# Performance work log

Hardware: AMD Instinct MI355X
Metric: run time of the kernel (lower is better)

## Reference

```python
import jax, jax.numpy as jnp
import numpy as np

B, H, W, D, O = 16, 128, 128, 64, 256

def setup_inputs() -> dict:
    key = jax.random.key(0)
    k1, k2 = jax.random.split(key)
    x = jax.random.normal(k1, (B, H, W, D), dtype=jnp.float32)
    omega = jax.random.normal(k2, (O, D), dtype=jnp.float32)  # prototypes, init N(0,1)
    return {"x": x, "omega": omega}

def reference(x, omega):
    # Squared L2 distance from each pixel feature to each prototype,
    x2 = jnp.sum(x * x, axis=-1, keepdims=True)          # [B,H,W,1]
    p2 = jnp.sum(omega * omega, axis=-1)                  # [O]
    xp = jnp.einsum('bhwd,od->bhwo', x, omega)            # [B,H,W,O]
    dist = x2 + p2 - 2.0 * xp                             # [B,H,W,O]
    # original stacks per-prototype [B,H,W,1] slices along dim=3 -> [B,H,W,O,1]
    return dist[..., None]
```

## Files before the change

### kernel.cpp

```cpp
#include <hip/hip_runtime.h>


typedef __attribute__((ext_vector_type(4))) float f32x4;
typedef __attribute__((ext_vector_type(16))) float f32x16;
typedef __attribute__((ext_vector_type(8))) short s16x8;
typedef __attribute__((ext_vector_type(4))) unsigned int u32x4;

constexpr int D_ = 64;
constexpr int O_ = 256;
constexpr int M_ = 16 * 128 * 128;
constexpr int ITERS = 2;
constexpr int PIX_PER_BLOCK = 4 * 32 * ITERS;
constexpr int NBLOCKS = M_ / PIX_PER_BLOCK;

__device__ __forceinline__ unsigned short f2bf(float f) {
    unsigned u = __builtin_bit_cast(unsigned, f);
    u += 0x7FFFu + ((u >> 16) & 1u);
    return (unsigned short)(u >> 16);
}

__global__ __launch_bounds__(256, 4) void dist_kernel(
    const float* __restrict__ x,
    const float* __restrict__ om,
    float* __restrict__ out)
{
    __shared__ u32x4 lfrag[32 * 64];
    __shared__ __align__(16) float lp2[O_];

    const int tid  = threadIdx.x;
    const int wave = tid >> 6;
    const int lane = tid & 63;
    const int p    = lane & 31;
    const int h    = lane >> 5;

#pragma unroll
    for (int tt = 0; tt < 2; ++tt) {
        const int T = wave * 2 + tt;
        float p2p = 0.f;
#pragma unroll
        for (int s = 0; s < 4; ++s) {
            const float* src = om + (T * 32 + p) * D_ + s * 16 + h * 8;
            f32x4 v0 = *(const f32x4*)(src);
            f32x4 v1 = *(const f32x4*)(src + 4);
            s16x8 f;
#pragma unroll
            for (int j = 0; j < 4; ++j) {
                f[j]     = (short)f2bf(v0[j]); p2p += v0[j] * v0[j];
                f[4 + j] = (short)f2bf(v1[j]); p2p += v1[j] * v1[j];
            }
            lfrag[(T * 4 + s) * 64 + lane] = __builtin_bit_cast(u32x4, f);
        }
        p2p += __shfl_xor(p2p, 32);
        if (lane < 32) lp2[T * 32 + p] = p2p;
    }
    __syncthreads();

    float p2r[8];
#pragma unroll
    for (int T = 0; T < 8; ++T) p2r[T] = lp2[T * 32 + p];

    const int pix0 = blockIdx.x * PIX_PER_BLOCK;

    for (int it = 0; it < ITERS; ++it) {
        const int rbase = pix0 + it * 128 + wave * 32;

        const float* xs = x + (size_t)(rbase + p) * D_ + h * 8;
        s16x8 Af[4];
        float x2p = 0.f;
#pragma unroll
        for (int s = 0; s < 4; ++s) {
            f32x4 a0 = *(const f32x4*)(xs + s * 16);
            f32x4 a1 = *(const f32x4*)(xs + s * 16 + 4);
#pragma unroll
            for (int j = 0; j < 4; ++j) {
                Af[s][j]     = (short)f2bf(a0[j]); x2p += a0[j] * a0[j];
                Af[s][4 + j] = (short)f2bf(a1[j]); x2p += a1[j] * a1[j];
            }
        }
        x2p += __shfl_xor(x2p, 32);

        float x2r[16];
#pragma unroll
        for (int reg = 0; reg < 16; ++reg)
            x2r[reg] = __shfl(x2p, (reg & 3) + 8 * (reg >> 2) + 4 * h);

        float* const obase = out + (size_t)(rbase + 4 * h) * O_ + p;

#pragma unroll
        for (int T = 0; T < 8; ++T) {
            f32x16 acc = {0.f, 0.f, 0.f, 0.f, 0.f, 0.f, 0.f, 0.f,
                          0.f, 0.f, 0.f, 0.f, 0.f, 0.f, 0.f, 0.f};
#pragma unroll
            for (int s = 0; s < 4; ++s) {
                s16x8 Bf = __builtin_bit_cast(s16x8, lfrag[(T * 4 + s) * 64 + lane]);
                acc = __builtin_amdgcn_mfma_f32_32x32x16_bf16(Af[s], Bf, acc, 0, 0, 0);
            }
#pragma unroll
            for (int reg = 0; reg < 16; ++reg) {
                const float val = (x2r[reg] + p2r[T]) - 2.f * acc[reg];
                obase[((reg & 3) + 8 * (reg >> 2)) * O_ + T * 32] = val;
            }
        }
    }
}

extern "C" void kernel_launch(void* const* d_in, const int* in_sizes, int n_in,
                              void* d_out, int out_size, void* d_ws, size_t ws_size,
                              hipStream_t stream) {
    const float* x  = (const float*)d_in[0];
    const float* om = (const float*)d_in[1];
    float* out = (float*)d_out;

    dist_kernel<<<dim3(NBLOCKS), dim3(256), 0, stream>>>(x, om, out);
}
```

Baseline: 74.01 us.

## Keep prototype fragments in registers and double-buffer x tiles through LDS

Each wave now owns two 32-prototype column tiles with their bf16 B fragments and norms held in registers, so the per-MFMA LDS reads of omega go away. Each block processes 32 pixels per iteration, with the whole block loading them coalesced into a padded, double-buffered LDS staging area using nontemporal loads. The next tile is prefetched during compute. The trade-off is a barrier per iteration, and every wave redundantly converts the same x rows to bf16 and recomputes their norms.

```diff
diff --git a/kernel.cpp b/kernel.cpp
--- a/kernel.cpp
+++ b/kernel.cpp
@@ -4,14 +4,15 @@
 typedef __attribute__((ext_vector_type(4))) float f32x4;
 typedef __attribute__((ext_vector_type(16))) float f32x16;
 typedef __attribute__((ext_vector_type(8))) short s16x8;
-typedef __attribute__((ext_vector_type(4))) unsigned int u32x4;
 
 constexpr int D_ = 64;
 constexpr int O_ = 256;
 constexpr int M_ = 16 * 128 * 128;
-constexpr int ITERS = 2;
-constexpr int PIX_PER_BLOCK = 4 * 32 * ITERS;
+constexpr int ITERS = 8;
+constexpr int PIX_PER_ITER = 32;
+constexpr int PIX_PER_BLOCK = ITERS * PIX_PER_ITER;
 constexpr int NBLOCKS = M_ / PIX_PER_BLOCK;
+constexpr int LROW = 68;
 
 __device__ __forceinline__ unsigned short f2bf(float f) {
     unsigned u = __builtin_bit_cast(unsigned, f);
@@ -24,8 +25,7 @@
     const float* __restrict__ om,
     float* __restrict__ out)
 {
-    __shared__ u32x4 lfrag[32 * 64];
-    __shared__ __align__(16) float lp2[O_];
+    __shared__ float xstg[2][32 * LROW];
 
     const int tid  = threadIdx.x;
     const int wave = tid >> 6;
@@ -33,6 +33,8 @@
     const int p    = lane & 31;
     const int h    = lane >> 5;
 
+    s16x8 Bf[2][4];
+    float p2r[2];
 #pragma unroll
     for (int tt = 0; tt < 2; ++tt) {
         const int T = wave * 2 + tt;
@@ -42,35 +44,48 @@
             const float* src = om + (T * 32 + p) * D_ + s * 16 + h * 8;
             f32x4 v0 = *(const f32x4*)(src);
             f32x4 v1 = *(const f32x4*)(src + 4);
-            s16x8 f;
 #pragma unroll
             for (int j = 0; j < 4; ++j) {
-                f[j]     = (short)f2bf(v0[j]); p2p += v0[j] * v0[j];
-                f[4 + j] = (short)f2bf(v1[j]); p2p += v1[j] * v1[j];
+                Bf[tt][s][j]     = (short)f2bf(v0[j]); p2p += v0[j] * v0[j];
+                Bf[tt][s][4 + j] = (short)f2bf(v1[j]); p2p += v1[j] * v1[j];
             }
-            lfrag[(T * 4 + s) * 64 + lane] = __builtin_bit_cast(u32x4, f);
         }
         p2p += __shfl_xor(p2p, 32);
-        if (lane < 32) lp2[T * 32 + p] = p2p;
+        p2r[tt] = p2p;
+    }
+
+    const size_t gbase = (size_t)blockIdx.x * PIX_PER_BLOCK * D_;
+    const int sr = tid >> 4;
+    const int sc = (tid & 15) * 4;
+
+    {
+        const float* src = x + gbase + tid * 4;
+        f32x4 v0 = __builtin_nontemporal_load((const f32x4*)(src));
+        f32x4 v1 = __builtin_nontemporal_load((const f32x4*)(src + 1024));
+        *(f32x4*)&xstg[0][sr * LROW + sc] = v0;
+        *(f32x4*)&xstg[0][(16 + sr) * LROW + sc] = v1;
     }
     __syncthreads();
 
-    float p2r[8];
-#pragma unroll
-    for (int T = 0; T < 8; ++T) p2r[T] = lp2[T * 32 + p];
+    for (int it = 0; it < ITERS; ++it) {
+        const int cur = it & 1, nxt = cur ^ 1;
+        const int rbase = blockIdx.x * PIX_PER_BLOCK + it * PIX_PER_ITER;
 
-    const int pix0 = blockIdx.x * PIX_PER_BLOCK;
+        f32x4 nv0, nv1;
+        const bool pf = (it + 1 < ITERS);
+        if (pf) {
+            const float* src = x + gbase + (size_t)(it + 1) * (PIX_PER_ITER * D_) + tid * 4;
+            nv0 = __builtin_nontemporal_load((const f32x4*)(src));
+            nv1 = __builtin_nontemporal_load((const f32x4*)(src + 1024));
+        }
 
-    for (int it = 0; it < ITERS; ++it) {
-        const int rbase = pix0 + it * 128 + wave * 32;
-
-        const float* xs = x + (size_t)(rbase + p) * D_ + h * 8;
+        const float* row = &xstg[cur][p * LROW + h * 8];
         s16x8 Af[4];
         float x2p = 0.f;
 #pragma unroll
         for (int s = 0; s < 4; ++s) {
-            f32x4 a0 = *(const f32x4*)(xs + s * 16);
-            f32x4 a1 = *(const f32x4*)(xs + s * 16 + 4);
+            f32x4 a0 = *(const f32x4*)(row + s * 16);
+            f32x4 a1 = *(const f32x4*)(row + s * 16 + 4);
 #pragma unroll
             for (int j = 0; j < 4; ++j) {
                 Af[s][j]     = (short)f2bf(a0[j]); x2p += a0[j] * a0[j];
@@ -84,23 +99,28 @@
         for (int reg = 0; reg < 16; ++reg)
             x2r[reg] = __shfl(x2p, (reg & 3) + 8 * (reg >> 2) + 4 * h);
 
-        float* const obase = out + (size_t)(rbase + 4 * h) * O_ + p;
-
 #pragma unroll
-        for (int T = 0; T < 8; ++T) {
+        for (int tt = 0; tt < 2; ++tt) {
+            const int T = wave * 2 + tt;
             f32x16 acc = {0.f, 0.f, 0.f, 0.f, 0.f, 0.f, 0.f, 0.f,
                           0.f, 0.f, 0.f, 0.f, 0.f, 0.f, 0.f, 0.f};
 #pragma unroll
-            for (int s = 0; s < 4; ++s) {
-                s16x8 Bf = __builtin_bit_cast(s16x8, lfrag[(T * 4 + s) * 64 + lane]);
-                acc = __builtin_amdgcn_mfma_f32_32x32x16_bf16(Af[s], Bf, acc, 0, 0, 0);
-            }
+            for (int s = 0; s < 4; ++s)
+                acc = __builtin_amdgcn_mfma_f32_32x32x16_bf16(Af[s], Bf[tt][s], acc, 0, 0, 0);
+
+            float* const obase = out + (size_t)(rbase + 4 * h) * O_ + T * 32 + p;
 #pragma unroll
             for (int reg = 0; reg < 16; ++reg) {
-                const float val = (x2r[reg] + p2r[T]) - 2.f * acc[reg];
-                obase[((reg & 3) + 8 * (reg >> 2)) * O_ + T * 32] = val;
+                const float val = (x2r[reg] + p2r[tt]) - 2.f * acc[reg];
+                obase[((reg & 3) + 8 * (reg >> 2)) * O_] = val;
             }
         }
+
+        if (pf) {
+            *(f32x4*)&xstg[nxt][sr * LROW + sc] = nv0;
+            *(f32x4*)&xstg[nxt][(16 + sr) * LROW + sc] = nv1;
+        }
+        __syncthreads();
     }
 }
 
```

Measured after the change: 69.53 us. -6.1%, faster.
